# Performance work log

Measured on AMD Instinct MI355X. Metric: run time of the kernel, lower is better.

## Reference

```python
import jax, jax.numpy as jnp
import numpy as np
import math

B, L, D, E, H = 8, 128, 512, 64, 8
SLOPE = 0.2
EPS = 1e-5


def setup_inputs() -> dict:
    key = jax.random.key(0)
    ks = jax.random.split(key, 10)
    s = 0.02
    x = jax.random.normal(ks[0], (B, L, D), jnp.float32)
    adj = jax.random.randint(ks[1], (B, L, L), 0, 2, jnp.int32)  # 0/1 adjacency
    e = jax.random.normal(ks[2], (B, L, L, E), jnp.float32)
    Wq = jax.random.normal(ks[3], (D, D), jnp.float32) * s
    Wkv = jax.random.normal(ks[4], (D, D), jnp.float32) * s
    We = jax.random.normal(ks[5], (E, D), jnp.float32) * s
    Wf = jax.random.normal(ks[6], (D, D), jnp.float32) * s
    bf = jnp.zeros((D,), jnp.float32)
    gamma = jnp.ones((D,), jnp.float32)
    beta = jnp.zeros((D,), jnp.float32)
    return {"x": x, "adj": adj, "e": e, "Wq": Wq, "Wkv": Wkv, "We": We,
            "Wf": Wf, "bf": bf, "gamma": gamma, "beta": beta}


def reference(x, adj, e, Wq, Wkv, We, Wf, bf, gamma, beta):
    C = D // H
    # projections
    q = (x @ Wq).reshape(B, L, H, C).transpose(0, 2, 1, 3)    # (B,H,L,C)
    kv = (x @ Wkv).reshape(B, L, H, C).transpose(0, 2, 1, 3)  # (B,H,L,C)
    ee = (e @ We).reshape(B, L, L, H, C).transpose(0, 3, 1, 2, 4)  # (B,H,Lq,Lk,C)
    # edge-modulated value/key: depends on both query and key position
    kve = kv[:, :, None, :, :] + ee                            # (B,H,Lq,Lk,C)
    # scores
    alpha = jnp.einsum('bhqc,bhqkc->bhqk', q, kve) / math.sqrt(C)
    alpha = jax.nn.leaky_relu(alpha, SLOPE)
    mask = (adj != 0)[:, None, :, :]                           # (B,1,Lq,Lk)
    alpha = jnp.where(mask, alpha, jnp.float32(-1e9))
    alpha = jax.nn.softmax(alpha, axis=-1)                     # over keys
    # weighted sum of edge-modulated values
    out = jnp.einsum('bhqk,bhqkc->bhqc', alpha, kve)           # (B,H,L,C)
    out = out.transpose(0, 2, 1, 3).reshape(B, L, D)
    # FFN: Linear -> LayerNorm -> ReLU
    out = out @ Wf + bf
    mu = out.mean(-1, keepdims=True)
    var = ((out - mu) ** 2).mean(-1, keepdims=True)
    out = (out - mu) / jnp.sqrt(var + EPS) * gamma + beta
    return jax.nn.relu(out)
```

## Files before the change

kernel.cpp:

```cpp
#include <hip/hip_runtime.h>
#include <hip/hip_bf16.h>
#include <math.h>

#define BB 8
#define LL 128
#define DD 512
#define EE 64
#define HH 8
#define CC 64
#define SLOPE 0.2f
#define EPS 1e-5f

typedef short bf16x8v __attribute__((ext_vector_type(8)));
typedef float f32x4v __attribute__((ext_vector_type(4)));

static __device__ __forceinline__ unsigned short f2bf(float f) {
    union { float f; unsigned u; } v; v.f = f;
    unsigned r = v.u + 0x7FFFu + ((v.u >> 16) & 1u);
    return (unsigned short)(r >> 16);
}

__global__ __launch_bounds__(256) void pack_all(
    const float* __restrict__ x, const float* __restrict__ Wq,
    const float* __restrict__ Wkv, const float* __restrict__ Wf,
    const float* __restrict__ We,
    unsigned short* __restrict__ xb, unsigned short* __restrict__ Wqkv_t,
    unsigned short* __restrict__ Wf_t, unsigned short* __restrict__ We_bf,
    unsigned short* __restrict__ WeT_bf)
{
    const int blk = blockIdx.x, tid = threadIdx.x;
    if (blk < 256) {
        const int j = blk * 512 + tid * 2;
        #pragma unroll
        for (int i = 0; i < 2; ++i) {
            const float4 v = ((const float4*)x)[j + i];
            ushort4 u; u.x = f2bf(v.x); u.y = f2bf(v.y); u.z = f2bf(v.z); u.w = f2bf(v.w);
            ((ushort4*)xb)[j + i] = u;
        }
    } else if (blk < 1024) {
        __shared__ float tile[32][33];
        const int matId = (blk - 256) >> 8;
        const int t = (blk - 256) & 255;
        const float* src = matId == 0 ? Wq : (matId == 1 ? Wkv : Wf);
        unsigned short* dst = matId == 0 ? Wqkv_t : (matId == 1 ? Wqkv_t + DD * DD : Wf_t);
        const int xx = tid & 31, yy = tid >> 5;
        const int r0 = (t >> 4) * 32, c0 = (t & 15) * 32;
        #pragma unroll
        for (int j = 0; j < 32; j += 8)
            tile[yy + j][xx] = src[(r0 + yy + j) * DD + c0 + xx];
        __syncthreads();
        #pragma unroll
        for (int j = 0; j < 32; j += 8)
            dst[(c0 + yy + j) * DD + r0 + xx] = f2bf(tile[xx][yy + j]);
    } else if (blk < 1040) {
        const int j = (blk - 1024) * 512 + tid * 2;
        #pragma unroll
        for (int i = 0; i < 2; ++i) {
            const float4 v = ((const float4*)We)[j + i];
            ushort4 u; u.x = f2bf(v.x); u.y = f2bf(v.y); u.z = f2bf(v.z); u.w = f2bf(v.w);
            ((ushort4*)We_bf)[j + i] = u;
        }
    } else {
        __shared__ float tile[32][33];
        const int t = blk - 1040;
        const int xx = tid & 31, yy = tid >> 5;
        const int r0 = (t >> 4) * 32, c0 = (t & 15) * 32;
        #pragma unroll
        for (int j = 0; j < 32; j += 8)
            tile[yy + j][xx] = We[(r0 + yy + j) * DD + c0 + xx];
        __syncthreads();
        #pragma unroll
        for (int j = 0; j < 32; j += 8)
            WeT_bf[(c0 + yy + j) * EE + r0 + xx] = f2bf(tile[xx][yy + j]);
    }
}

__global__ __launch_bounds__(256) void proj_gemm(
    const unsigned short* __restrict__ A, const unsigned short* __restrict__ Bm,
    unsigned short* __restrict__ Q_bf, unsigned short* __restrict__ KV_bf,
    unsigned short* __restrict__ KVT_bf)
{
    const int wave = threadIdx.x >> 6, lane = threadIdx.x & 63;
    const int quad = lane >> 4, l16 = lane & 15;
    const int m0 = blockIdx.y * 64 + wave * 16;
    const int n0 = blockIdx.x * 64;
    const bf16x8v* Ap = (const bf16x8v*)(A + (m0 + l16) * DD) + quad;
    const bf16x8v* Bp = (const bf16x8v*)(Bm + (n0 + l16) * DD) + quad;
    f32x4v acc0 = {0.f,0.f,0.f,0.f}, acc1 = acc0, acc2 = acc0, acc3 = acc0;
    #pragma unroll 4
    for (int k = 0; k < 16; ++k) {
        const bf16x8v a = Ap[k * 4];
        acc0 = __builtin_amdgcn_mfma_f32_16x16x32_bf16(a, Bp[k * 4       ], acc0, 0, 0, 0);
        acc1 = __builtin_amdgcn_mfma_f32_16x16x32_bf16(a, Bp[k * 4 + 1024], acc1, 0, 0, 0);
        acc2 = __builtin_amdgcn_mfma_f32_16x16x32_bf16(a, Bp[k * 4 + 2048], acc2, 0, 0, 0);
        acc3 = __builtin_amdgcn_mfma_f32_16x16x32_bf16(a, Bp[k * 4 + 3072], acc3, 0, 0, 0);
    }
    const f32x4v accs[4] = {acc0, acc1, acc2, acc3};
    const int gm0 = m0 + quad * 4;
    #pragma unroll
    for (int t = 0; t < 4; ++t) {
        const int gn = n0 + t * 16 + l16;
        const int mat = gn >> 9, d = gn & 511, h = d >> 6, c = d & 63;
        unsigned short* dst = mat ? KV_bf : Q_bf;
        ushort4 pk;
        pk.x = f2bf(accs[t][0]); pk.y = f2bf(accs[t][1]);
        pk.z = f2bf(accs[t][2]); pk.w = f2bf(accs[t][3]);
        dst[(gm0 + 0) * DD + d] = pk.x;
        dst[(gm0 + 1) * DD + d] = pk.y;
        dst[(gm0 + 2) * DD + d] = pk.z;
        dst[(gm0 + 3) * DD + d] = pk.w;
        if (mat) {
            const int b = gm0 >> 7, l0 = gm0 & 127;
            *(ushort4*)&KVT_bf[(((b * HH + h) * CC + c) << 7) + l0] = pk;
        }
    }
}

__global__ __launch_bounds__(256) void qk_t_gemm(
    const unsigned short* __restrict__ Q_bf, const unsigned short* __restrict__ KV_bf,
    const unsigned short* __restrict__ We_bf,
    float* __restrict__ S1, unsigned short* __restrict__ T_bf)
{
    const int wave = threadIdx.x >> 6, lane = threadIdx.x & 63;
    const int quad = lane >> 4, l16 = lane & 15;
    const int bid = blockIdx.x;
    f32x4v acc[4];
    #pragma unroll
    for (int t = 0; t < 4; ++t) acc[t] = (f32x4v){0.f,0.f,0.f,0.f};

    if (bid < 256) {
        const int batch = bid >> 2, sub = bid & 3;
        const int b = batch >> 3, h = batch & 7;
        const int q0 = (sub >> 1) * 64 + wave * 16;
        const int k0 = (sub & 1) * 64;
        const unsigned short* Ap = Q_bf + (b * LL + q0 + l16) * DD + h * CC + quad * 8;
        #pragma unroll
        for (int ks = 0; ks < 2; ++ks) {
            const bf16x8v a = *(const bf16x8v*)(Ap + ks * 32);
            #pragma unroll
            for (int t = 0; t < 4; ++t) {
                const bf16x8v bb = *(const bf16x8v*)(KV_bf + (b * LL + k0 + t * 16 + l16) * DD + h * CC + quad * 8 + ks * 32);
                acc[t] = __builtin_amdgcn_mfma_f32_16x16x32_bf16(a, bb, acc[t], 0, 0, 0);
            }
        }
        #pragma unroll
        for (int t = 0; t < 4; ++t)
            #pragma unroll
            for (int r = 0; r < 4; ++r)
                S1[((batch * LL + q0 + quad * 4 + r) << 7) + k0 + t * 16 + l16] = acc[t][r];
    } else {
        const int bid2 = bid - 256;
        const int h = bid2 >> 4;
        const int m0 = (bid2 & 15) * 64 + wave * 16;
        const unsigned short* Ap = Q_bf + (m0 + l16) * DD + h * CC + quad * 8;
        #pragma unroll
        for (int ks = 0; ks < 2; ++ks) {
            const bf16x8v a = *(const bf16x8v*)(Ap + ks * 32);
            #pragma unroll
            for (int t = 0; t < 4; ++t) {
                const bf16x8v bb = *(const bf16x8v*)(We_bf + (t * 16 + l16) * DD + h * CC + quad * 8 + ks * 32);
                acc[t] = __builtin_amdgcn_mfma_f32_16x16x32_bf16(a, bb, acc[t], 0, 0, 0);
            }
        }
        #pragma unroll
        for (int t = 0; t < 4; ++t)
            #pragma unroll
            for (int r = 0; r < 4; ++r)
                T_bf[(m0 + quad * 4 + r) * DD + h * CC + t * 16 + l16] = f2bf(acc[t][r]);
    }
}

#define ES 72
#define ETS 136
__global__ __launch_bounds__(256) void attn_fused(
    const float* __restrict__ e, const int* __restrict__ adj,
    const float* __restrict__ S1, const unsigned short* __restrict__ T_bf,
    unsigned short* __restrict__ P1, unsigned short* __restrict__ G_bf)
{
    __shared__ unsigned short lds_e[LL * ES];
    __shared__ unsigned short lds_eT[EE * ETS];
    __shared__ float s_lds[HH * 132];
    __shared__ unsigned short p_bf[HH * ETS];

    const int bq = blockIdx.x;
    const int b = bq >> 7, q = bq & 127;
    const int tid = threadIdx.x;
    const int wave = tid >> 6, lane = tid & 63, quad = lane >> 4, l16 = lane & 15;

    const float4* e4 = (const float4*)(e + (size_t)bq * (LL * EE));
    #pragma unroll
    for (int rep = 0; rep < 8; ++rep) {
        const int j = rep * 256 + tid;
        const float4 v = e4[j];
        const int k = j >> 4, x0 = (j & 15) * 4;
        ushort4 u; u.x = f2bf(v.x); u.y = f2bf(v.y); u.z = f2bf(v.z); u.w = f2bf(v.w);
        *(ushort4*)&lds_e[k * ES + x0] = u;
        lds_eT[(x0    ) * ETS + k] = u.x;
        lds_eT[(x0 + 1) * ETS + k] = u.y;
        lds_eT[(x0 + 2) * ETS + k] = u.z;
        lds_eT[(x0 + 3) * ETS + k] = u.w;
    }
    __syncthreads();

    const int hh = l16 < 8 ? l16 : 7;
    const unsigned short* Trow = T_bf + bq * DD + hh * CC + quad * 8;
    const bf16x8v tb0 = *(const bf16x8v*)(Trow);
    const bf16x8v tb1 = *(const bf16x8v*)(Trow + 32);
    f32x4v sacc[2];
    #pragma unroll
    for (int mt = 0; mt < 2; ++mt) {
        sacc[mt] = (f32x4v){0.f,0.f,0.f,0.f};
        const int kb = wave * 32 + mt * 16;
        const bf16x8v a0 = *(const bf16x8v*)&lds_e[(kb + l16) * ES + quad * 8];
        const bf16x8v a1 = *(const bf16x8v*)&lds_e[(kb + l16) * ES + 32 + quad * 8];
        sacc[mt] = __builtin_amdgcn_mfma_f32_16x16x32_bf16(a0, tb0, sacc[mt], 0, 0, 0);
        sacc[mt] = __builtin_amdgcn_mfma_f32_16x16x32_bf16(a1, tb1, sacc[mt], 0, 0, 0);
    }
    if (l16 < 8) {
        #pragma unroll
        for (int mt = 0; mt < 2; ++mt) {
            const int kk0 = wave * 32 + mt * 16 + quad * 4;
            const float4 s1v = *(const float4*)&S1[(((b * HH + l16) * LL + q) << 7) + kk0];
            const int4 av = *(const int4*)&adj[bq * LL + kk0];
            float sv[4] = {s1v.x, s1v.y, s1v.z, s1v.w};
            const int am[4] = {av.x, av.y, av.z, av.w};
            float4 o;
            float* op = (float*)&o;
            #pragma unroll
            for (int r = 0; r < 4; ++r) {
                float sc = (sv[r] + sacc[mt][r]) * 0.125f;
                sc = (sc >= 0.f) ? sc : SLOPE * sc;
                op[r] = (am[r] == 0) ? -1e9f : sc;
            }
            *(float4*)&s_lds[l16 * 132 + kk0] = o;
        }
    }
    __syncthreads();

    {
        const int h = tid >> 5, t5 = tid & 31;
        float m = -INFINITY;
        #pragma unroll
        for (int i = 0; i < 4; ++i) m = fmaxf(m, s_lds[h * 132 + t5 + i * 32]);
        #pragma unroll
        for (int off = 16; off > 0; off >>= 1) m = fmaxf(m, __shfl_down(m, off, 32));
        m = __shfl(m, 0, 32);
        const int k0 = t5 * 4;
        float ev[4];
        #pragma unroll
        for (int i = 0; i < 4; ++i) ev[i] = expf(s_lds[h * 132 + k0 + i] - m);
        float l = ev[0] + ev[1] + ev[2] + ev[3];
        #pragma unroll
        for (int off = 16; off > 0; off >>= 1) l += __shfl_down(l, off, 32);
        l = __shfl(l, 0, 32);
        const float inv = 1.f / l;
        ushort4 pk;
        pk.x = f2bf(ev[0] * inv); pk.y = f2bf(ev[1] * inv);
        pk.z = f2bf(ev[2] * inv); pk.w = f2bf(ev[3] * inv);
        *(ushort4*)&p_bf[h * ETS + k0] = pk;
        *(ushort4*)&P1[(((b * HH + h) * LL + q) << 7) + k0] = pk;
    }
    __syncthreads();

    {
        const int hr = l16 < 8 ? l16 : 0;
        f32x4v g = {0.f,0.f,0.f,0.f};
        #pragma unroll
        for (int ks = 0; ks < 4; ++ks) {
            const bf16x8v a  = *(const bf16x8v*)&p_bf[hr * ETS + ks * 32 + quad * 8];
            const bf16x8v bb = *(const bf16x8v*)&lds_eT[(wave * 16 + l16) * ETS + ks * 32 + quad * 8];
            g = __builtin_amdgcn_mfma_f32_16x16x32_bf16(a, bb, g, 0, 0, 0);
        }
        if (quad < 2) {
            #pragma unroll
            for (int r = 0; r < 4; ++r)
                G_bf[bq * DD + (quad * 4 + r) * CC + wave * 16 + l16] = f2bf(g[r]);
        }
    }
}

__global__ __launch_bounds__(256) void pv_gemm(
    const unsigned short* __restrict__ P1, const unsigned short* __restrict__ KVT_bf,
    float* __restrict__ O1)
{
    const int wave = threadIdx.x >> 6, lane = threadIdx.x & 63;
    const int quad = lane >> 4, l16 = lane & 15;
    const int batch = blockIdx.x >> 1;
    const int q0 = (blockIdx.x & 1) * 64 + wave * 16;
    const int b = batch >> 3, h = batch & 7;
    f32x4v acc[4];
    #pragma unroll
    for (int t = 0; t < 4; ++t) acc[t] = (f32x4v){0.f,0.f,0.f,0.f};
    const unsigned short* Ap = P1 + ((batch * LL + q0 + l16) << 7) + quad * 8;
    #pragma unroll
    for (int ks = 0; ks < 4; ++ks) {
        const bf16x8v a = *(const bf16x8v*)(Ap + ks * 32);
        #pragma unroll
        for (int t = 0; t < 4; ++t) {
            const bf16x8v bb = *(const bf16x8v*)(KVT_bf + (((batch * CC + t * 16 + l16)) << 7) + quad * 8 + ks * 32);
            acc[t] = __builtin_amdgcn_mfma_f32_16x16x32_bf16(a, bb, acc[t], 0, 0, 0);
        }
    }
    #pragma unroll
    for (int t = 0; t < 4; ++t)
        #pragma unroll
        for (int r = 0; r < 4; ++r)
            O1[(b * LL + q0 + quad * 4 + r) * DD + h * CC + t * 16 + l16] = acc[t][r];
}

__global__ __launch_bounds__(256) void o2_gemm(
    const unsigned short* __restrict__ G_bf, const unsigned short* __restrict__ WeT_bf,
    const float* __restrict__ O1, unsigned short* __restrict__ attn_bf)
{
    const int wave = threadIdx.x >> 6, lane = threadIdx.x & 63;
    const int quad = lane >> 4, l16 = lane & 15;
    const int h = blockIdx.x >> 4;
    const int m0 = (blockIdx.x & 15) * 64 + wave * 16;
    f32x4v acc[4];
    #pragma unroll
    for (int t = 0; t < 4; ++t) acc[t] = (f32x4v){0.f,0.f,0.f,0.f};
    const unsigned short* Ap = G_bf + (m0 + l16) * DD + h * CC + quad * 8;
    #pragma unroll
    for (int ks = 0; ks < 2; ++ks) {
        const bf16x8v a = *(const bf16x8v*)(Ap + ks * 32);
        #pragma unroll
        for (int t = 0; t < 4; ++t) {
            const bf16x8v bb = *(const bf16x8v*)(WeT_bf + (h * CC + t * 16 + l16) * EE + quad * 8 + ks * 32);
            acc[t] = __builtin_amdgcn_mfma_f32_16x16x32_bf16(a, bb, acc[t], 0, 0, 0);
        }
    }
    #pragma unroll
    for (int t = 0; t < 4; ++t) {
        const int d = h * CC + t * 16 + l16;
        #pragma unroll
        for (int r = 0; r < 4; ++r) {
            const int row = m0 + quad * 4 + r;
            attn_bf[row * DD + d] = f2bf(acc[t][r] + O1[row * DD + d]);
        }
    }
}

__global__ __launch_bounds__(256) void ffn_gemm(
    const unsigned short* __restrict__ A, const unsigned short* __restrict__ Bm,
    const float* __restrict__ bfv, float* __restrict__ vals)
{
    const int wave = threadIdx.x >> 6, lane = threadIdx.x & 63;
    const int quad = lane >> 4, l16 = lane & 15;
    const int m0 = blockIdx.y * 64 + wave * 16;
    const int n0 = blockIdx.x * 64;
    const bf16x8v* Ap = (const bf16x8v*)(A + (m0 + l16) * DD) + quad;
    const bf16x8v* Bp = (const bf16x8v*)(Bm + (n0 + l16) * DD) + quad;
    f32x4v acc0 = {0.f,0.f,0.f,0.f}, acc1 = acc0, acc2 = acc0, acc3 = acc0;
    #pragma unroll 4
    for (int k = 0; k < 16; ++k) {
        const bf16x8v a = Ap[k * 4];
        acc0 = __builtin_amdgcn_mfma_f32_16x16x32_bf16(a, Bp[k * 4       ], acc0, 0, 0, 0);
        acc1 = __builtin_amdgcn_mfma_f32_16x16x32_bf16(a, Bp[k * 4 + 1024], acc1, 0, 0, 0);
        acc2 = __builtin_amdgcn_mfma_f32_16x16x32_bf16(a, Bp[k * 4 + 2048], acc2, 0, 0, 0);
        acc3 = __builtin_amdgcn_mfma_f32_16x16x32_bf16(a, Bp[k * 4 + 3072], acc3, 0, 0, 0);
    }
    const f32x4v accs[4] = {acc0, acc1, acc2, acc3};
    #pragma unroll
    for (int t = 0; t < 4; ++t) {
        const int gn = n0 + t * 16 + l16;
        const float bias = bfv[gn];
        #pragma unroll
        for (int r = 0; r < 4; ++r)
            vals[(m0 + quad * 4 + r) * DD + gn] = accs[t][r] + bias;
    }
}

__global__ __launch_bounds__(256) void ln_kernel(
    const float* __restrict__ vals, const float* __restrict__ gamma,
    const float* __restrict__ beta, float* __restrict__ out)
{
    __shared__ float red[8];
    __shared__ float stats[2];
    const int row = blockIdx.x;
    const int tid = threadIdx.x;
    const float v0 = vals[row * DD + tid];
    const float v1 = vals[row * DD + tid + 256];
    float ls = v0 + v1;
    float lss = v0 * v0 + v1 * v1;
    #pragma unroll
    for (int off = 32; off > 0; off >>= 1) {
        ls += __shfl_down(ls, off);
        lss += __shfl_down(lss, off);
    }
    const int wid = tid >> 6;
    if ((tid & 63) == 0) { red[wid * 2] = ls; red[wid * 2 + 1] = lss; }
    __syncthreads();
    if (tid == 0) {
        float ts = 0.f, tss = 0.f;
        for (int w = 0; w < 4; ++w) { ts += red[w * 2]; tss += red[w * 2 + 1]; }
        const float mu = ts / (float)DD;
        const float var = tss / (float)DD - mu * mu;
        stats[0] = mu;
        stats[1] = rsqrtf(var + EPS);
    }
    __syncthreads();
    const float mu = stats[0], rsig = stats[1];
    const float o0 = (v0 - mu) * rsig * gamma[tid] + beta[tid];
    const float o1 = (v1 - mu) * rsig * gamma[tid + 256] + beta[tid + 256];
    out[row * DD + tid] = fmaxf(o0, 0.f);
    out[row * DD + tid + 256] = fmaxf(o1, 0.f);
}

extern "C" void kernel_launch(void* const* d_in, const int* in_sizes, int n_in,
                              void* d_out, int out_size, void* d_ws, size_t ws_size,
                              hipStream_t stream)
{
    const float* x    = (const float*)d_in[0];
    const int*   adj  = (const int*)  d_in[1];
    const float* e    = (const float*)d_in[2];
    const float* Wq   = (const float*)d_in[3];
    const float* Wkv  = (const float*)d_in[4];
    const float* We   = (const float*)d_in[5];
    const float* Wf   = (const float*)d_in[6];
    const float* bf   = (const float*)d_in[7];
    const float* gam  = (const float*)d_in[8];
    const float* bet  = (const float*)d_in[9];
    float* out = (float*)d_out;

    const int MROW = BB * LL;
    char* w = (char*)d_ws;
    unsigned short* Q_bf   = (unsigned short*)(w);
    unsigned short* KV_bf  = (unsigned short*)(w + (1u  << 20));
    unsigned short* KVT_bf = (unsigned short*)(w + (2u  << 20));
    float*          S1     = (float*)         (w + (3u  << 20));
    unsigned short* T_bf   = (unsigned short*)(w + (7u  << 20));
    unsigned short* P1     = (unsigned short*)(w + (8u  << 20));
    unsigned short* G_bf   = (unsigned short*)(w + (10u << 20));
    float*          O1     = (float*)         (w + (11u << 20));
    float*          vals   = (float*)         (w + (13u << 20));
    unsigned short* xb     = (unsigned short*)(w + (15u << 20));
    unsigned short* Wqkv_t = (unsigned short*)(w + (16u << 20));
    unsigned short* Wf_t   = (unsigned short*)(w + (17u << 20));
    unsigned short* We_bf  = (unsigned short*)(w + (17u << 20) + (512u << 10));
    unsigned short* WeT_bf = (unsigned short*)(w + (17u << 20) + (576u << 10));

    pack_all<<<1072, 256, 0, stream>>>(x, Wq, Wkv, Wf, We, xb, Wqkv_t, Wf_t, We_bf, WeT_bf);
    proj_gemm<<<dim3(16, 16), 256, 0, stream>>>(xb, Wqkv_t, Q_bf, KV_bf, KVT_bf);
    qk_t_gemm<<<384, 256, 0, stream>>>(Q_bf, KV_bf, We_bf, S1, T_bf);
    attn_fused<<<MROW, 256, 0, stream>>>(e, adj, S1, T_bf, P1, G_bf);
    pv_gemm<<<128, 256, 0, stream>>>(P1, KVT_bf, O1);
    o2_gemm<<<128, 256, 0, stream>>>(G_bf, WeT_bf, O1, (unsigned short*)Q_bf );
    ffn_gemm<<<dim3(8, 16), 256, 0, stream>>>((unsigned short*)Q_bf, Wf_t, bf, vals);
    ln_kernel<<<MROW, 256, 0, stream>>>(vals, gam, bet, out);
}
```

Before: 140.7 us.

## Fold Q·We into projection GEMM, fuse PV with O2, retile small GEMMs

Precomputes Wq·We^T per head inside the pack kernel so T is produced by the main projection GEMM as extra output columns. This removes the separate T computation from the QK kernel. PV and the edge-output GEMM are merged into one kernel accumulating into the same registers, which drops the fp32 O1 round trip and one launch. The QK, PV and FFN GEMMs are retiled to smaller per-wave tiles to put more blocks in flight. The change also switches expf to __expf and adjusts an LDS pad. T now carries an extra bf16 rounding of the folded weight, which changes numerics slightly.

```diff
diff --git a/kernel.cpp b/kernel.cpp
--- a/kernel.cpp
+++ b/kernel.cpp
@@ -20,6 +20,17 @@
     return (unsigned short)(r >> 16);
 }
 
+static __device__ __forceinline__ bf16x8v ld8f_bf(const float* __restrict__ p) {
+    const float4 v0 = *(const float4*)p;
+    const float4 v1 = *(const float4*)(p + 4);
+    bf16x8v r;
+    r[0] = (short)f2bf(v0.x); r[1] = (short)f2bf(v0.y);
+    r[2] = (short)f2bf(v0.z); r[3] = (short)f2bf(v0.w);
+    r[4] = (short)f2bf(v1.x); r[5] = (short)f2bf(v1.y);
+    r[6] = (short)f2bf(v1.z); r[7] = (short)f2bf(v1.w);
+    return r;
+}
+
 __global__ __launch_bounds__(256) void pack_all(
     const float* __restrict__ x, const float* __restrict__ Wq,
     const float* __restrict__ Wkv, const float* __restrict__ Wf,
@@ -60,7 +71,7 @@
             ushort4 u; u.x = f2bf(v.x); u.y = f2bf(v.y); u.z = f2bf(v.z); u.w = f2bf(v.w);
             ((ushort4*)We_bf)[j + i] = u;
         }
-    } else {
+    } else if (blk < 1072) {
         __shared__ float tile[32][33];
         const int t = blk - 1040;
         const int xx = tid & 31, yy = tid >> 5;
@@ -72,13 +83,39 @@
         #pragma unroll
         for (int j = 0; j < 32; j += 8)
             WeT_bf[(c0 + yy + j) * EE + r0 + xx] = f2bf(tile[xx][yy + j]);
+    } else {
+        const int blk2 = blk - 1072;
+        const int h = blk2 >> 3;
+        const int d0 = (blk2 & 7) * 64;
+        const int wave = tid >> 6, lane = tid & 63;
+        const int quad = lane >> 4, l16 = lane & 15;
+        const int dr = d0 + wave * 16;
+        f32x4v acc[4];
+        #pragma unroll
+        for (int t = 0; t < 4; ++t) acc[t] = (f32x4v){0.f,0.f,0.f,0.f};
+        #pragma unroll
+        for (int ks = 0; ks < 2; ++ks) {
+            const bf16x8v a = ld8f_bf(Wq + (dr + l16) * DD + h * CC + quad * 8 + ks * 32);
+            #pragma unroll
+            for (int t = 0; t < 4; ++t) {
+                const bf16x8v bb = ld8f_bf(We + (t * 16 + l16) * DD + h * CC + quad * 8 + ks * 32);
+                acc[t] = __builtin_amdgcn_mfma_f32_16x16x32_bf16(a, bb, acc[t], 0, 0, 0);
+            }
+        }
+        #pragma unroll
+        for (int t = 0; t < 4; ++t) {
+            const int nrow = 1024 + h * CC + t * 16 + l16;
+            #pragma unroll
+            for (int r = 0; r < 4; ++r)
+                Wqkv_t[nrow * DD + dr + quad * 4 + r] = f2bf(acc[t][r]);
+        }
     }
 }
 
 __global__ __launch_bounds__(256) void proj_gemm(
     const unsigned short* __restrict__ A, const unsigned short* __restrict__ Bm,
     unsigned short* __restrict__ Q_bf, unsigned short* __restrict__ KV_bf,
-    unsigned short* __restrict__ KVT_bf)
+    unsigned short* __restrict__ KVT_bf, unsigned short* __restrict__ T_bf)
 {
     const int wave = threadIdx.x >> 6, lane = threadIdx.x & 63;
     const int quad = lane >> 4, l16 = lane & 15;
@@ -101,77 +138,54 @@
     for (int t = 0; t < 4; ++t) {
         const int gn = n0 + t * 16 + l16;
         const int mat = gn >> 9, d = gn & 511, h = d >> 6, c = d & 63;
-        unsigned short* dst = mat ? KV_bf : Q_bf;
         ushort4 pk;
         pk.x = f2bf(accs[t][0]); pk.y = f2bf(accs[t][1]);
         pk.z = f2bf(accs[t][2]); pk.w = f2bf(accs[t][3]);
+        unsigned short* dst = mat == 0 ? Q_bf : (mat == 1 ? KV_bf : T_bf);
         dst[(gm0 + 0) * DD + d] = pk.x;
         dst[(gm0 + 1) * DD + d] = pk.y;
         dst[(gm0 + 2) * DD + d] = pk.z;
         dst[(gm0 + 3) * DD + d] = pk.w;
-        if (mat) {
+        if (mat == 1) {
             const int b = gm0 >> 7, l0 = gm0 & 127;
             *(ushort4*)&KVT_bf[(((b * HH + h) * CC + c) << 7) + l0] = pk;
         }
     }
 }
 
-__global__ __launch_bounds__(256) void qk_t_gemm(
+__global__ __launch_bounds__(256) void qk_s1(
     const unsigned short* __restrict__ Q_bf, const unsigned short* __restrict__ KV_bf,
-    const unsigned short* __restrict__ We_bf,
-    float* __restrict__ S1, unsigned short* __restrict__ T_bf)
+    float* __restrict__ S1)
 {
     const int wave = threadIdx.x >> 6, lane = threadIdx.x & 63;
     const int quad = lane >> 4, l16 = lane & 15;
     const int bid = blockIdx.x;
-    f32x4v acc[4];
-    #pragma unroll
-    for (int t = 0; t < 4; ++t) acc[t] = (f32x4v){0.f,0.f,0.f,0.f};
-
-    if (bid < 256) {
-        const int batch = bid >> 2, sub = bid & 3;
-        const int b = batch >> 3, h = batch & 7;
-        const int q0 = (sub >> 1) * 64 + wave * 16;
-        const int k0 = (sub & 1) * 64;
-        const unsigned short* Ap = Q_bf + (b * LL + q0 + l16) * DD + h * CC + quad * 8;
-        #pragma unroll
-        for (int ks = 0; ks < 2; ++ks) {
-            const bf16x8v a = *(const bf16x8v*)(Ap + ks * 32);
-            #pragma unroll
-            for (int t = 0; t < 4; ++t) {
-                const bf16x8v bb = *(const bf16x8v*)(KV_bf + (b * LL + k0 + t * 16 + l16) * DD + h * CC + quad * 8 + ks * 32);
-                acc[t] = __builtin_amdgcn_mfma_f32_16x16x32_bf16(a, bb, acc[t], 0, 0, 0);
-            }
-        }
-        #pragma unroll
-        for (int t = 0; t < 4; ++t)
-            #pragma unroll
-            for (int r = 0; r < 4; ++r)
-                S1[((batch * LL + q0 + quad * 4 + r) << 7) + k0 + t * 16 + l16] = acc[t][r];
-    } else {
-        const int bid2 = bid - 256;
-        const int h = bid2 >> 4;
-        const int m0 = (bid2 & 15) * 64 + wave * 16;
-        const unsigned short* Ap = Q_bf + (m0 + l16) * DD + h * CC + quad * 8;
-        #pragma unroll
-        for (int ks = 0; ks < 2; ++ks) {
-            const bf16x8v a = *(const bf16x8v*)(Ap + ks * 32);
-            #pragma unroll
-            for (int t = 0; t < 4; ++t) {
-                const bf16x8v bb = *(const bf16x8v*)(We_bf + (t * 16 + l16) * DD + h * CC + quad * 8 + ks * 32);
-                acc[t] = __builtin_amdgcn_mfma_f32_16x16x32_bf16(a, bb, acc[t], 0, 0, 0);
-            }
-        }
-        #pragma unroll
-        for (int t = 0; t < 4; ++t)
-            #pragma unroll
-            for (int r = 0; r < 4; ++r)
-                T_bf[(m0 + quad * 4 + r) * DD + h * CC + t * 16 + l16] = f2bf(acc[t][r]);
-    }
+    const int batch = bid >> 3;
+    const int sub = bid & 7;
+    const int b = batch >> 3, h = batch & 7;
+    const int q0 = (sub >> 1) * 32 + (wave >> 1) * 16;
+    const int k0 = (sub & 1) * 64 + (wave & 1) * 32;
+    f32x4v acc[2];
+    acc[0] = (f32x4v){0.f,0.f,0.f,0.f}; acc[1] = acc[0];
+    const unsigned short* Ap = Q_bf + (b * LL + q0 + l16) * DD + h * CC + quad * 8;
+    #pragma unroll
+    for (int ks = 0; ks < 2; ++ks) {
+        const bf16x8v a = *(const bf16x8v*)(Ap + ks * 32);
+        #pragma unroll
+        for (int t = 0; t < 2; ++t) {
+            const bf16x8v bb = *(const bf16x8v*)(KV_bf + (b * LL + k0 + t * 16 + l16) * DD + h * CC + quad * 8 + ks * 32);
+            acc[t] = __builtin_amdgcn_mfma_f32_16x16x32_bf16(a, bb, acc[t], 0, 0, 0);
+        }
+    }
+    #pragma unroll
+    for (int t = 0; t < 2; ++t)
+        #pragma unroll
+        for (int r = 0; r < 4; ++r)
+            S1[((batch * LL + q0 + quad * 4 + r) << 7) + k0 + t * 16 + l16] = acc[t][r];
 }
 
 #define ES 72
-#define ETS 136
+#define ETS 138
 __global__ __launch_bounds__(256) void attn_fused(
     const float* __restrict__ e, const int* __restrict__ adj,
     const float* __restrict__ S1, const unsigned short* __restrict__ T_bf,
@@ -248,7 +262,7 @@
         const int k0 = t5 * 4;
         float ev[4];
         #pragma unroll
-        for (int i = 0; i < 4; ++i) ev[i] = expf(s_lds[h * 132 + k0 + i] - m);
+        for (int i = 0; i < 4; ++i) ev[i] = __expf(s_lds[h * 132 + k0 + i] - m);
         float l = ev[0] + ev[1] + ev[2] + ev[3];
         #pragma unroll
         for (int off = 16; off > 0; off >>= 1) l += __shfl_down(l, off, 32);
@@ -279,64 +293,50 @@
     }
 }
 
-__global__ __launch_bounds__(256) void pv_gemm(
+__global__ __launch_bounds__(256) void pv_o2_gemm(
     const unsigned short* __restrict__ P1, const unsigned short* __restrict__ KVT_bf,
-    float* __restrict__ O1)
+    const unsigned short* __restrict__ G_bf, const unsigned short* __restrict__ WeT_bf,
+    unsigned short* __restrict__ attn_bf)
 {
     const int wave = threadIdx.x >> 6, lane = threadIdx.x & 63;
     const int quad = lane >> 4, l16 = lane & 15;
-    const int batch = blockIdx.x >> 1;
-    const int q0 = (blockIdx.x & 1) * 64 + wave * 16;
+    const int batch = blockIdx.x >> 2;
+    const int qt = blockIdx.x & 3;
+    const int q0 = qt * 32 + (wave >> 1) * 16;
+    const int c0 = (wave & 1) * 32;
     const int b = batch >> 3, h = batch & 7;
-    f32x4v acc[4];
-    #pragma unroll
-    for (int t = 0; t < 4; ++t) acc[t] = (f32x4v){0.f,0.f,0.f,0.f};
+    f32x4v acc[2];
+    acc[0] = (f32x4v){0.f,0.f,0.f,0.f}; acc[1] = acc[0];
+
     const unsigned short* Ap = P1 + ((batch * LL + q0 + l16) << 7) + quad * 8;
     #pragma unroll
     for (int ks = 0; ks < 4; ++ks) {
         const bf16x8v a = *(const bf16x8v*)(Ap + ks * 32);
         #pragma unroll
-        for (int t = 0; t < 4; ++t) {
-            const bf16x8v bb = *(const bf16x8v*)(KVT_bf + (((batch * CC + t * 16 + l16)) << 7) + quad * 8 + ks * 32);
+        for (int t = 0; t < 2; ++t) {
+            const bf16x8v bb = *(const bf16x8v*)(KVT_bf + ((batch * CC + c0 + t * 16 + l16) << 7) + quad * 8 + ks * 32);
             acc[t] = __builtin_amdgcn_mfma_f32_16x16x32_bf16(a, bb, acc[t], 0, 0, 0);
         }
     }
-    #pragma unroll
-    for (int t = 0; t < 4; ++t)
+
+    const int gm = b * LL + q0;
+    const unsigned short* Gp = G_bf + (gm + l16) * DD + h * CC + quad * 8;
+    #pragma unroll
+    for (int ks = 0; ks < 2; ++ks) {
+        const bf16x8v a = *(const bf16x8v*)(Gp + ks * 32);
+        #pragma unroll
+        for (int t = 0; t < 2; ++t) {
+            const bf16x8v bb = *(const bf16x8v*)(WeT_bf + (h * CC + c0 + t * 16 + l16) * EE + quad * 8 + ks * 32);
+            acc[t] = __builtin_amdgcn_mfma_f32_16x16x32_bf16(a, bb, acc[t], 0, 0, 0);
+        }
+    }
+
+    #pragma unroll
+    for (int t = 0; t < 2; ++t) {
+        const int d = h * CC + c0 + t * 16 + l16;
         #pragma unroll
         for (int r = 0; r < 4; ++r)
-            O1[(b * LL + q0 + quad * 4 + r) * DD + h * CC + t * 16 + l16] = acc[t][r];
-}
-
-__global__ __launch_bounds__(256) void o2_gemm(
-    const unsigned short* __restrict__ G_bf, const unsigned short* __restrict__ WeT_bf,
-    const float* __restrict__ O1, unsigned short* __restrict__ attn_bf)
-{
-    const int wave = threadIdx.x >> 6, lane = threadIdx.x & 63;
-    const int quad = lane >> 4, l16 = lane & 15;
-    const int h = blockIdx.x >> 4;
-    const int m0 = (blockIdx.x & 15) * 64 + wave * 16;
-    f32x4v acc[4];
-    #pragma unroll
-    for (int t = 0; t < 4; ++t) acc[t] = (f32x4v){0.f,0.f,0.f,0.f};
-    const unsigned short* Ap = G_bf + (m0 + l16) * DD + h * CC + quad * 8;
-    #pragma unroll
-    for (int ks = 0; ks < 2; ++ks) {
-        const bf16x8v a = *(const bf16x8v*)(Ap + ks * 32);
-        #pragma unroll
-        for (int t = 0; t < 4; ++t) {
-            const bf16x8v bb = *(const bf16x8v*)(WeT_bf + (h * CC + t * 16 + l16) * EE + quad * 8 + ks * 32);
-            acc[t] = __builtin_amdgcn_mfma_f32_16x16x32_bf16(a, bb, acc[t], 0, 0, 0);
-        }
-    }
-    #pragma unroll
-    for (int t = 0; t < 4; ++t) {
-        const int d = h * CC + t * 16 + l16;
-        #pragma unroll
-        for (int r = 0; r < 4; ++r) {
-            const int row = m0 + quad * 4 + r;
-            attn_bf[row * DD + d] = f2bf(acc[t][r] + O1[row * DD + d]);
-        }
+            attn_bf[(gm + quad * 4 + r) * DD + d] = f2bf(acc[t][r]);
     }
 }
 
@@ -346,22 +346,20 @@
 {
     const int wave = threadIdx.x >> 6, lane = threadIdx.x & 63;
     const int quad = lane >> 4, l16 = lane & 15;
-    const int m0 = blockIdx.y * 64 + wave * 16;
-    const int n0 = blockIdx.x * 64;
+    const int m0 = blockIdx.y * 32 + (wave >> 1) * 16;
+    const int n0 = blockIdx.x * 64 + (wave & 1) * 32;
     const bf16x8v* Ap = (const bf16x8v*)(A + (m0 + l16) * DD) + quad;
     const bf16x8v* Bp = (const bf16x8v*)(Bm + (n0 + l16) * DD) + quad;
-    f32x4v acc0 = {0.f,0.f,0.f,0.f}, acc1 = acc0, acc2 = acc0, acc3 = acc0;
+    f32x4v acc0 = {0.f,0.f,0.f,0.f}, acc1 = acc0;
     #pragma unroll 4
     for (int k = 0; k < 16; ++k) {
         const bf16x8v a = Ap[k * 4];
         acc0 = __builtin_amdgcn_mfma_f32_16x16x32_bf16(a, Bp[k * 4       ], acc0, 0, 0, 0);
         acc1 = __builtin_amdgcn_mfma_f32_16x16x32_bf16(a, Bp[k * 4 + 1024], acc1, 0, 0, 0);
-        acc2 = __builtin_amdgcn_mfma_f32_16x16x32_bf16(a, Bp[k * 4 + 2048], acc2, 0, 0, 0);
-        acc3 = __builtin_amdgcn_mfma_f32_16x16x32_bf16(a, Bp[k * 4 + 3072], acc3, 0, 0, 0);
-    }
-    const f32x4v accs[4] = {acc0, acc1, acc2, acc3};
-    #pragma unroll
-    for (int t = 0; t < 4; ++t) {
+    }
+    const f32x4v accs[2] = {acc0, acc1};
+    #pragma unroll
+    for (int t = 0; t < 2; ++t) {
         const int gn = n0 + t * 16 + l16;
         const float bias = bfv[gn];
         #pragma unroll
@@ -431,20 +429,18 @@
     unsigned short* T_bf   = (unsigned short*)(w + (7u  << 20));
     unsigned short* P1     = (unsigned short*)(w + (8u  << 20));
     unsigned short* G_bf   = (unsigned short*)(w + (10u << 20));
-    float*          O1     = (float*)         (w + (11u << 20));
-    float*          vals   = (float*)         (w + (13u << 20));
-    unsigned short* xb     = (unsigned short*)(w + (15u << 20));
-    unsigned short* Wqkv_t = (unsigned short*)(w + (16u << 20));
-    unsigned short* Wf_t   = (unsigned short*)(w + (17u << 20));
-    unsigned short* We_bf  = (unsigned short*)(w + (17u << 20) + (512u << 10));
-    unsigned short* WeT_bf = (unsigned short*)(w + (17u << 20) + (576u << 10));
-
-    pack_all<<<1072, 256, 0, stream>>>(x, Wq, Wkv, Wf, We, xb, Wqkv_t, Wf_t, We_bf, WeT_bf);
-    proj_gemm<<<dim3(16, 16), 256, 0, stream>>>(xb, Wqkv_t, Q_bf, KV_bf, KVT_bf);
-    qk_t_gemm<<<384, 256, 0, stream>>>(Q_bf, KV_bf, We_bf, S1, T_bf);
+    float*          vals   = (float*)         (w + (11u << 20));
+    unsigned short* xb     = (unsigned short*)(w + (13u << 20));
+    unsigned short* Wqkv_t = (unsigned short*)(w + (14u << 20));
+    unsigned short* Wf_t   = (unsigned short*)(w + (15u << 20) + (512u << 10));
+    unsigned short* We_bf  = (unsigned short*)(w + (16u << 20));
+    unsigned short* WeT_bf = (unsigned short*)(w + (16u << 20) + (64u << 10));
+
+    pack_all<<<1136, 256, 0, stream>>>(x, Wq, Wkv, Wf, We, xb, Wqkv_t, Wf_t, We_bf, WeT_bf);
+    proj_gemm<<<dim3(24, 16), 256, 0, stream>>>(xb, Wqkv_t, Q_bf, KV_bf, KVT_bf, T_bf);
+    qk_s1<<<512, 256, 0, stream>>>(Q_bf, KV_bf, S1);
     attn_fused<<<MROW, 256, 0, stream>>>(e, adj, S1, T_bf, P1, G_bf);
-    pv_gemm<<<128, 256, 0, stream>>>(P1, KVT_bf, O1);
-    o2_gemm<<<128, 256, 0, stream>>>(G_bf, WeT_bf, O1, (unsigned short*)Q_bf );
-    ffn_gemm<<<dim3(8, 16), 256, 0, stream>>>((unsigned short*)Q_bf, Wf_t, bf, vals);
+    pv_o2_gemm<<<256, 256, 0, stream>>>(P1, KVT_bf, G_bf, WeT_bf, (unsigned short*)Q_bf);
+    ffn_gemm<<<dim3(8, 32), 256, 0, stream>>>((unsigned short*)Q_bf, Wf_t, bf, vals);
     ln_kernel<<<MROW, 256, 0, stream>>>(vals, gam, bet, out);
 }
```

After: 141.0 us (median of 2 runs). Within noise of the previous version (+0.2%).
